# Optimization experiments

Measured on AMD Instinct MI355X. Metric: run time of the kernel, lower is better.

Reference implementation:

```python
import jax, jax.numpy as jnp
import numpy as np

B, LP, LQ, H = 32, 2048, 512, 1024

def setup_inputs() -> dict:
    key = jax.random.key(0)
    k1, k2, k3, k4 = jax.random.split(key, 4)
    p_encode = jax.random.normal(k1, (B, LP, H), dtype=jnp.float32)
    q_encode = jax.random.normal(k2, (B, LQ, H), dtype=jnp.float32)
    # nn.Linear(H, H): weight [out, in], bias [out]
    bound = 1.0 / np.sqrt(H)
    G_weight = jax.random.uniform(k3, (H, H), dtype=jnp.float32, minval=-bound, maxval=bound)
    G_bias = jax.random.uniform(k4, (H,), dtype=jnp.float32, minval=-bound, maxval=bound)
    return {"p_encode": p_encode, "q_encode": q_encode, "G_weight": G_weight, "G_bias": G_bias}

def reference(p_encode, q_encode, G_weight, G_bias):
    # q_project = transpose(G(q_encode), -2, -1): [B, H, LQ]
    q_proj = jnp.einsum('bqh,oh->bqo', q_encode, G_weight) + G_bias  # [B, LQ, H]
    # att_matrix = bmm(p_encode, q_project^T): [B, LP, LQ]
    att = jnp.einsum('bph,bqh->bpq', p_encode, q_proj)
    # m_p = softmax over LQ (dim=-1) @ q_encode -> [B, LP, H]
    m_p = jnp.einsum('bpq,bqh->bph', jax.nn.softmax(att, axis=-1), q_encode)
    # m_q = softmax over LP (dim=-2), transposed, @ p_encode -> [B, LQ, H]
    m_q = jnp.einsum('bpq,bph->bqh', jax.nn.softmax(att, axis=-2), p_encode)
    return (m_p, m_q)
```

## Files before the change

### kernel.cpp

```cpp
#include <hip/hip_runtime.h>

typedef _Float16 half_t;
typedef _Float16 f16x8 __attribute__((ext_vector_type(8)));
typedef _Float16 f16x4 __attribute__((ext_vector_type(4)));
typedef float    f32x4 __attribute__((ext_vector_type(4)));
typedef float    f32x16 __attribute__((ext_vector_type(16)));

typedef const __attribute__((address_space(1))) void cg_void;
typedef __attribute__((address_space(3))) void lds_void;

#define BB 32
#define LP 2048
#define LQ 512
#define HH 1024

enum { M_QPROJ = 0, M_OUT32 = 1 };

__global__ void cvt16_k(const float* __restrict__ w, half_t* __restrict__ o) {
  long i = ((long)blockIdx.x * 256 + threadIdx.x) * 4;
  f32x4 v = *(const f32x4*)(w + i);
  f16x4 h;
  h[0] = (half_t)v[0]; h[1] = (half_t)v[1]; h[2] = (half_t)v[2]; h[3] = (half_t)v[3];
  *(f16x4*)(o + i) = h;
}

__global__ __launch_bounds__(256) void cvt2_k(const float* __restrict__ qe,
                                              half_t* __restrict__ q16o,
                                              half_t* __restrict__ qT16o,
                                              const float* __restrict__ pe,
                                              half_t* __restrict__ p16o,
                                              half_t* __restrict__ pT16o) {
  __shared__ half_t tile[64 * 64];
  const int byg = blockIdx.y;
  const float* in; half_t* rm; half_t* tr; int R, r0;
  if (byg < 8) { in = qe; rm = q16o; tr = qT16o; R = LQ; r0 = byg * 64; }
  else         { in = pe; rm = p16o; tr = pT16o; R = LP; r0 = (byg - 8) * 64; }
  const int C = HH;
  const long zb = blockIdx.z;
  const float* src = in + zb * (long)R * C;
  half_t* dstT = tr + zb * (long)C * R;
  half_t* dstR = rm + zb * (long)R * C;
  const int c0 = blockIdx.x * 64;
  const int t = threadIdx.x;
  const int cl = (t & 15) * 4;
  const int rl = t >> 4;
#pragma unroll
  for (int rr = 0; rr < 4; rr++) {
    int r = rr * 16 + rl;
    f32x4 v = *(const f32x4*)(src + (long)(r0 + r) * C + c0 + cl);
    f16x4 h;
#pragma unroll
    for (int j = 0; j < 4; j++) {
      h[j] = (half_t)v[j];
      int c = cl + j;
      tile[c * 64 + (r ^ (((c >> 3) & 7) << 3))] = h[j];
    }
    *(f16x4*)(dstR + (long)(r0 + r) * C + c0 + cl) = h;
  }
  __syncthreads();
  const int c = t >> 2;
  const int rch = (t & 3) * 16;
  const int m = (c >> 3) & 7;
  const int B0 = c * 64 + (rch ^ ((m << 3) & 48));
  const int hi = (m & 1) << 3;
  f16x8 g0 = *(const f16x8*)&tile[B0 + hi];
  f16x8 g1 = *(const f16x8*)&tile[B0 + (8 ^ hi)];
  half_t* dp = dstT + (long)(c0 + c) * R + r0 + rch;
  *(f16x8*)dp = g0;
  *(f16x8*)(dp + 8) = g1;
}

__global__ __launch_bounds__(256) void cfin_k(const float* __restrict__ pmg,
                                              const float* __restrict__ psg,
                                              float* __restrict__ cmax,
                                              float* __restrict__ cinv) {
  long i = (long)blockIdx.x * 256 + threadIdx.x;
  long b = i / LQ, q = i - b * LQ;
  const float* mp = pmg + (b * 16) * LQ + q;
  const float* sp = psg + (b * 16) * LQ + q;
  float m = -3e38f, s = 0.f;
#pragma unroll
  for (int t = 0; t < 16; t++) {
    float mm = mp[(long)t * LQ], ss = sp[(long)t * LQ];
    float nm = fmaxf(m, mm);
    s = s * __expf(m - nm) + ss * __expf(mm - nm);
    m = nm;
  }
  cmax[i] = m;
  cinv[i] = 1.f / s;
}

__global__ __launch_bounds__(256) void pq_k(const half_t* __restrict__ E,
                                            half_t* __restrict__ out,
                                            const float* __restrict__ pmg,
                                            const float* __restrict__ cmax,
                                            const float* __restrict__ cinv) {
  __shared__ half_t tile[64 * 64];
  const long zb = blockIdx.z;
  const half_t* src = E + zb * (long)LP * LQ;
  half_t* dst = out + zb * (long)LQ * LP;
  const int r0 = blockIdx.y * 64, c0 = blockIdx.x * 64;
  const int tIdx = r0 >> 7;
  const int t = threadIdx.x;
  const int cl = (t & 15) * 4;
  const int rl = t >> 4;
  f32x4 tm = *(const f32x4*)(pmg + ((long)zb * 16 + tIdx) * LQ + c0 + cl);
  f32x4 cm = *(const f32x4*)(cmax + (long)zb * LQ + c0 + cl);
  f32x4 ci = *(const f32x4*)(cinv + (long)zb * LQ + c0 + cl);
  float sc[4];
#pragma unroll
  for (int j = 0; j < 4; j++) sc[j] = __expf(tm[j] - cm[j]) * ci[j];
#pragma unroll
  for (int rr = 0; rr < 4; rr++) {
    int r = rr * 16 + rl;
    f16x4 v = *(const f16x4*)(src + (long)(r0 + r) * LQ + c0 + cl);
#pragma unroll
    for (int j = 0; j < 4; j++) {
      float x = (float)v[j] * sc[j];
      int c = cl + j;
      tile[c * 64 + (r ^ (((c >> 3) & 7) << 3))] = (half_t)x;
    }
  }
  __syncthreads();
  const int c = t >> 2;
  const int rch = (t & 3) * 16;
  const int m = (c >> 3) & 7;
  const int B0 = c * 64 + (rch ^ ((m << 3) & 48));
  const int hi = (m & 1) << 3;
  f16x8 g0 = *(const f16x8*)&tile[B0 + hi];
  f16x8 g1 = *(const f16x8*)&tile[B0 + (8 ^ hi)];
  half_t* dp = dst + (long)(c0 + c) * LP + r0 + rch;
  *(f16x8*)dp = g0;
  *(f16x8*)(dp + 8) = g1;
}

template<int ROWS>
__device__ __forceinline__ void stage_op(const half_t* src, int ld,
                                         half_t* lds_base, int wid, int lane) {
  const int goff = (((lane & 3) ^ ((lane >> 3) & 3)) << 3);
#pragma unroll
  for (int j = 0; j < ROWS / 128; ++j) {
    int row = j * 128 + wid * 16 + (lane >> 2);
    const half_t* g = src + (long)row * ld + goff;
    __builtin_amdgcn_global_load_lds((cg_void*)g,
        (lds_void*)(lds_base + j * 4096 + wid * 512), 16, 0, 0);
  }
}

__device__ __forceinline__ void xcd_swz(long lid, long nwg, long& out) {
  const long q8 = nwg >> 3, r8 = nwg & 7;
  const long xcd = lid & 7, rest = lid >> 3;
  out = (xcd < r8 ? xcd * (q8 + 1) : r8 * (q8 + 1) + (xcd - r8) * q8) + rest;
}

__global__ __launch_bounds__(512, 2) void attf_k(
    const half_t* __restrict__ Ap, const half_t* __restrict__ Bp,
    half_t* __restrict__ PpO, half_t* __restrict__ EO,
    float* __restrict__ pmg, float* __restrict__ psg) {
  __shared__ __align__(16) half_t As[3 * 4096];
  __shared__ __align__(16) half_t Bs[3 * 16384];
  __shared__ float rmL[4][128];
  __shared__ float cmL[2][512];
  __shared__ float rsL[4][128];
  __shared__ float csL[2][512];

  const int nby = gridDim.y;
  long lid;
  xcd_swz(blockIdx.y + (long)nby * blockIdx.z, (long)nby * gridDim.z, lid);
  const int by = (int)(lid % nby);
  const int bz = (int)(lid / nby);

  const int t0 = threadIdx.x;
  const int lane = t0 & 63;
  const int wid = t0 >> 6;
  const int wm = wid >> 2, wn = wid & 3;
  const int m0 = by * 128;

  const half_t* Abase = Ap + ((long)bz * LP + m0) * HH;
  const half_t* Bbase = Bp + (long)bz * LQ * HH;

  const int c5 = lane & 31, hi = lane >> 5;
  const int sx = (c5 >> 1) & 3;
  const int ofs0 = c5 * 32 + ((hi ^ sx) << 3);
  const int ofs1 = c5 * 32 + (((2 | hi) ^ sx) << 3);

  f32x16 acc[2][4] = {};
  const int NT = HH / 32;

#pragma unroll
  for (int tt = 0; tt < 2; ++tt) {
    stage_op<128>(Abase + tt * 32, HH, As + tt * 4096, wid, lane);
    stage_op<512>(Bbase + tt * 32, HH, Bs + tt * 16384, wid, lane);
  }

  for (int t = 0; t < NT; ++t) {
    if (t + 1 < NT) asm volatile("s_waitcnt vmcnt(5)" ::: "memory");
    else            asm volatile("s_waitcnt vmcnt(0)" ::: "memory");
    __builtin_amdgcn_s_barrier();
    asm volatile("" ::: "memory");

    const half_t* Au = As + (t % 3) * 4096;
    const half_t* Bu = Bs + (t % 3) * 16384;
    f16x8 af[2][2], bf[4][2];
#pragma unroll
    for (int mf = 0; mf < 2; ++mf) {
      const half_t* p = Au + (wm * 64 + mf * 32) * 32;
      af[mf][0] = *(const f16x8*)(p + ofs0);
      af[mf][1] = *(const f16x8*)(p + ofs1);
    }
#pragma unroll
    for (int nf = 0; nf < 4; ++nf) {
      const half_t* p = Bu + (wn * 128 + nf * 32) * 32;
      bf[nf][0] = *(const f16x8*)(p + ofs0);
      bf[nf][1] = *(const f16x8*)(p + ofs1);
    }
    if (t + 2 < NT) {
      const int u2 = (t + 2) % 3;
      stage_op<128>(Abase + (t + 2) * 32, HH, As + u2 * 4096, wid, lane);
      stage_op<512>(Bbase + (t + 2) * 32, HH, Bs + u2 * 16384, wid, lane);
    }
    __builtin_amdgcn_s_setprio(1);
#pragma unroll
    for (int mf = 0; mf < 2; ++mf)
#pragma unroll
      for (int nf = 0; nf < 4; ++nf) {
        acc[mf][nf] = __builtin_amdgcn_mfma_f32_32x32x16_f16(af[mf][0], bf[nf][0], acc[mf][nf], 0, 0, 0);
        acc[mf][nf] = __builtin_amdgcn_mfma_f32_32x32x16_f16(af[mf][1], bf[nf][1], acc[mf][nf], 0, 0, 0);
      }
    __builtin_amdgcn_s_setprio(0);
  }

  float rmv[2][16], cmv[4];
#pragma unroll
  for (int m = 0; m < 2; ++m)
#pragma unroll
    for (int r = 0; r < 16; ++r) {
      float v = fmaxf(fmaxf(acc[m][0][r], acc[m][1][r]), fmaxf(acc[m][2][r], acc[m][3][r]));
#pragma unroll
      for (int o = 1; o < 32; o <<= 1) v = fmaxf(v, __shfl_xor(v, o, 64));
      rmv[m][r] = v;
    }
#pragma unroll
  for (int n = 0; n < 4; ++n) {
    float v = acc[0][n][0];
#pragma unroll
    for (int m = 0; m < 2; ++m)
#pragma unroll
      for (int r = 0; r < 16; ++r) v = fmaxf(v, acc[m][n][r]);
    v = fmaxf(v, __shfl_xor(v, 32, 64));
    cmv[n] = v;
  }
  if (c5 < 16) {
#pragma unroll
    for (int m = 0; m < 2; ++m)
      rmL[wn][wm * 64 + m * 32 + (c5 & 3) + 8 * (c5 >> 2) + 4 * hi] = rmv[m][c5];
  }
  if (hi == 0) {
#pragma unroll
    for (int n = 0; n < 4; ++n) cmL[wm][wn * 128 + n * 32 + c5] = cmv[n];
  }
  __syncthreads();
  if (t0 < 128)
    rmL[0][t0] = fmaxf(fmaxf(rmL[0][t0], rmL[1][t0]), fmaxf(rmL[2][t0], rmL[3][t0]));
  {
    float cm2 = fmaxf(cmL[0][t0 & 511], cmL[1][t0 & 511]);
    cmL[0][t0 & 511] = cm2;
    pmg[((long)bz * 16 + by) * LQ + (t0 & 511)] = cm2;
  }
  __syncthreads();
#pragma unroll
  for (int m = 0; m < 2; ++m)
#pragma unroll
    for (int r = 0; r < 16; ++r)
      rmv[m][r] = rmL[0][wm * 64 + m * 32 + (r & 3) + 8 * (r >> 2) + 4 * hi];
#pragma unroll
  for (int n = 0; n < 4; ++n) cmv[n] = cmL[0][wn * 128 + n * 32 + c5];

  half_t* EB = EO + (long)bz * LP * LQ;
  float csW[4] = {0.f, 0.f, 0.f, 0.f};
  float rowS[2][16];
#pragma unroll
  for (int m = 0; m < 2; ++m)
#pragma unroll
    for (int r = 0; r < 16; ++r) {
      long grow = (long)(m0 + wm * 64 + m * 32 + (r & 3) + 8 * (r >> 2) + 4 * hi) * LQ;
      float s = 0.f;
#pragma unroll
      for (int n = 0; n < 4; ++n) {
        float a = acc[m][n][r];
        float e = __expf(a - cmv[n]);
        float p = __expf(a - rmv[m][r]);
        csW[n] += e;
        EB[grow + wn * 128 + n * 32 + c5] = (half_t)e;
        acc[m][n][r] = p;
        s += p;
      }
#pragma unroll
      for (int o = 1; o < 32; o <<= 1) s += __shfl_xor(s, o, 64);
      rowS[m][r] = s;
    }
#pragma unroll
  for (int n = 0; n < 4; ++n) csW[n] += __shfl_xor(csW[n], 32, 64);
  if (c5 < 16) {
#pragma unroll
    for (int m = 0; m < 2; ++m)
      rsL[wn][wm * 64 + m * 32 + (c5 & 3) + 8 * (c5 >> 2) + 4 * hi] = rowS[m][c5];
  }
  if (hi == 0) {
#pragma unroll
    for (int n = 0; n < 4; ++n) csL[wm][wn * 128 + n * 32 + c5] = csW[n];
  }
  __syncthreads();
  if (t0 < 128)
    rsL[0][t0] = 1.f / (rsL[0][t0] + rsL[1][t0] + rsL[2][t0] + rsL[3][t0]);
  psg[((long)bz * 16 + by) * LQ + (t0 & 511)] = csL[0][t0 & 511] + csL[1][t0 & 511];
  __syncthreads();

  half_t* PpB = PpO + (long)bz * LP * LQ;
#pragma unroll
  for (int m = 0; m < 2; ++m)
#pragma unroll
    for (int r = 0; r < 16; ++r) {
      int row = wm * 64 + m * 32 + (r & 3) + 8 * (r >> 2) + 4 * hi;
      long grow = (long)(m0 + row) * LQ;
      float ri = rsL[0][row];
#pragma unroll
      for (int n = 0; n < 4; ++n)
        PpB[grow + wn * 128 + n * 32 + c5] = (half_t)(acc[m][n][r] * ri);
    }
}

__device__ __forceinline__ void stage_half(const half_t* src, int ld, int k0,
                                           half_t* slot, int half_id, int wid, int lane) {
#pragma unroll
  for (int j = 0; j < 2; ++j) {
    int c = j * 512 + wid * 64 + lane;
    int lr = c >> 3, sl = c & 7;
    int gr = (lr & 63) + half_id * 64 + (lr >> 6) * 128;
    const half_t* g = src + (long)gr * ld + k0 + (((sl ^ (lr & 7))) << 3);
    __builtin_amdgcn_global_load_lds((cg_void*)g,
        (lds_void*)(slot + j * 4096 + wid * 512), 16, 0, 0);
  }
}

__device__ __forceinline__ void stage_s(int s, const half_t* Ab, const half_t* Bb,
                                        int lda, int ldb, half_t* lds, int NT,
                                        int wid, int lane) {
  int ts = s >> 2;
  if (ts >= NT) return;
  int kind = s & 3;
  half_t* slot = lds + (s & 7) * 8192;
  int k0 = ts * 64;
  if (kind == 0)      stage_half(Ab, lda, k0, slot, 0, wid, lane);
  else if (kind == 1) stage_half(Bb, ldb, k0, slot, 0, wid, lane);
  else if (kind == 2) stage_half(Bb, ldb, k0, slot, 1, wid, lane);
  else                stage_half(Ab, lda, k0, slot, 1, wid, lane);
}

template<int MODE>
__device__ __forceinline__ void core8p(const half_t* __restrict__ Ab,
                                       const half_t* __restrict__ Bb,
                                       void* __restrict__ cB,
                                       const float* __restrict__ biasB,
                                       int lda, int ldb, int ldc, int K,
                                       half_t* lds) {
  const int t0 = threadIdx.x;
  const int lane = t0 & 63;
  const int wid = t0 >> 6;
  const int wm = wid >> 2, wn = wid & 3;
  const int fr = lane & 15, fs = lane >> 4;

  f32x4 acc[8][4] = {};
  const int NT = K >> 6;

#pragma unroll
  for (int s = 0; s < 6; ++s) stage_s(s, Ab, Bb, lda, ldb, lds, NT, wid, lane);
  asm volatile("s_waitcnt vmcnt(6)" ::: "memory");
  __builtin_amdgcn_s_barrier();
  asm volatile("" ::: "memory");

  for (int t = 0; t < NT; ++t) {
    const int base4 = 4 * t;
    const half_t* slotA0 = lds + ((base4) & 7) * 8192;
    const half_t* slotB0 = lds + ((base4 + 1) & 7) * 8192;
    const half_t* slotB1 = lds + ((base4 + 2) & 7) * 8192;
    const half_t* slotA1 = lds + ((base4 + 3) & 7) * 8192;
    f16x8 bf[4][2];
#pragma unroll
    for (int p = 0; p < 4; ++p) {
      f16x8 af[2][2];
      const half_t* aslot = (p < 2) ? slotA0 : slotA1;
      const int lrbase = wm * 64 + (p & 1) * 32;
#pragma unroll
      for (int i = 0; i < 2; ++i) {
        int lr = lrbase + i * 16 + fr;
#pragma unroll
        for (int kh = 0; kh < 2; ++kh)
          af[i][kh] = *(const f16x8*)&aslot[lr * 64 + (((fs + 4 * kh) ^ (lr & 7)) << 3)];
      }
      if (p == 0) {
        const half_t* bslot = (wn & 1) ? slotB1 : slotB0;
#pragma unroll
        for (int nf = 0; nf < 4; ++nf) {
          int lr = (wn >> 1) * 64 + nf * 16 + fr;
#pragma unroll
          for (int kh = 0; kh < 2; ++kh)
            bf[nf][kh] = *(const f16x8*)&bslot[lr * 64 + (((fs + 4 * kh) ^ (lr & 7)) << 3)];
        }
      }
      stage_s(base4 + p + 6, Ab, Bb, lda, ldb, lds, NT, wid, lane);
      if (t + 2 < NT) {
        asm volatile("s_waitcnt vmcnt(6)" ::: "memory");
      } else if (t + 2 == NT) {
        if (p < 2)       asm volatile("s_waitcnt vmcnt(6)" ::: "memory");
        else if (p == 2) asm volatile("s_waitcnt vmcnt(4)" ::: "memory");
        else             asm volatile("s_waitcnt vmcnt(2)" ::: "memory");
      } else {
        asm volatile("s_waitcnt vmcnt(0)" ::: "memory");
      }
      __builtin_amdgcn_s_barrier();
      asm volatile("s_waitcnt lgkmcnt(0)" ::: "memory");
      __builtin_amdgcn_sched_barrier(0);
      __builtin_amdgcn_s_setprio(1);
#pragma unroll
      for (int kh = 0; kh < 2; ++kh)
#pragma unroll
        for (int i = 0; i < 2; ++i)
#pragma unroll
          for (int nf = 0; nf < 4; ++nf)
            acc[p * 2 + i][nf] =
                __builtin_amdgcn_mfma_f32_16x16x32_f16(af[i][kh], bf[nf][kh], acc[p * 2 + i][nf], 0, 0, 0);
      __builtin_amdgcn_s_setprio(0);
      __builtin_amdgcn_s_barrier();
      asm volatile("" ::: "memory");
    }
  }

  const int r0 = fs * 4;
#pragma unroll
  for (int nf = 0; nf < 4; ++nf) {
    int col = wn * 64 + nf * 16 + fr;
    float bv = 0.f;
    if constexpr (MODE == M_QPROJ) bv = biasB[col];
#pragma unroll
    for (int mf = 0; mf < 8; ++mf) {
      int row = wm * 128 + (mf >> 2) * 64 + ((mf >> 1) & 1) * 32 + (mf & 1) * 16 + r0;
#pragma unroll
      for (int j = 0; j < 4; j++) {
        if constexpr (MODE == M_QPROJ)
          ((half_t*)cB)[(long)(row + j) * ldc + col] = (half_t)(acc[mf][nf][j] + bv);
        else
          ((float*)cB)[(long)(row + j) * ldc + col] = acc[mf][nf][j];
      }
    }
  }
}

__global__ __launch_bounds__(512, 1) void gemmq_k(const half_t* __restrict__ q16,
                                                  const half_t* __restrict__ w16,
                                                  half_t* __restrict__ qpj,
                                                  const float* __restrict__ Gb) {
  __shared__ __align__(16) half_t lds[8 * 8192];
  long lid;
  xcd_swz(blockIdx.x + 4L * blockIdx.y, 4L * gridDim.y, lid);
  const int bx = (int)(lid % 4);
  const int by = (int)(lid / 4);
  core8p<M_QPROJ>(q16 + (long)(by * 256) * HH,
                  w16 + (long)(bx * 256) * HH,
                  qpj + (long)(by * 256) * HH + bx * 256,
                  Gb + bx * 256, HH, HH, HH, HH, lds);
}

__global__ __launch_bounds__(512, 1) void gemm2_k(
    const half_t* __restrict__ Pp, const half_t* __restrict__ qT16, float* __restrict__ m_p,
    const half_t* __restrict__ Pq, const half_t* __restrict__ pT16, float* __restrict__ m_q) {
  __shared__ __align__(16) half_t lds[8 * 8192];
  long lid;
  xcd_swz(blockIdx.x + 4L * (blockIdx.y + 10L * blockIdx.z), 4L * 10 * 32, lid);
  const int bx = (int)(lid % 4);
  const long tmp = lid / 4;
  const int by = (int)(tmp % 10);
  const int bz = (int)(tmp / 10);

  if (by < 2) {
    core8p<M_OUT32>(Pq + (long)bz * LQ * LP + (long)(by * 256) * LP,
                    pT16 + (long)bz * HH * LP + (long)(bx * 256) * LP,
                    m_q + (long)bz * LQ * HH + (long)(by * 256) * HH + bx * 256,
                    nullptr, LP, LP, HH, LP, lds);
  } else {
    const int py = by - 2;
    core8p<M_OUT32>(Pp + (long)bz * LP * LQ + (long)(py * 256) * LQ,
                    qT16 + (long)bz * HH * LQ + (long)(bx * 256) * LQ,
                    m_p + (long)bz * LP * HH + (long)(py * 256) * HH + bx * 256,
                    nullptr, LQ, LQ, HH, LQ, lds);
  }
}

extern "C" void kernel_launch(void* const* d_in, const int* in_sizes, int n_in,
                              void* d_out, int out_size, void* d_ws, size_t ws_size,
                              hipStream_t stream) {
  const float* p_enc = (const float*)d_in[0];
  const float* q_enc = (const float*)d_in[1];
  const float* Gw    = (const float*)d_in[2];
  const float* Gb    = (const float*)d_in[3];
  float* m_p = (float*)d_out;
  float* m_q = m_p + (long)BB * LP * HH;

  half_t* w16   = (half_t*)d_ws;
  half_t* q16   = w16 + (long)HH * HH;
  half_t* qT16  = q16 + (long)BB * LQ * HH;
  half_t* qpj16 = qT16 + (long)BB * HH * LQ;
  half_t* p16   = qpj16 + (long)BB * LQ * HH;
  half_t* pT16  = p16 + (long)BB * LP * HH;
  half_t* Pp    = pT16 + (long)BB * HH * LP;
  half_t* Ebuf  = Pp + (long)BB * LP * LQ;
  half_t* Pq    = Ebuf + (long)BB * LP * LQ;
  float*  cmaxb = (float*)(Pq + (long)BB * LQ * LP);
  float*  cinvb = cmaxb + (long)BB * LQ;
  float*  pmg   = cinvb + (long)BB * LQ;
  float*  psg   = pmg + (long)BB * 16 * LQ;

  cvt16_k<<<HH * HH / 1024, 256, 0, stream>>>(Gw, w16);

  cvt2_k<<<dim3(HH / 64, 40, BB), 256, 0, stream>>>(q_enc, q16, qT16, p_enc, p16, pT16);

  gemmq_k<<<dim3(4, 64, 1), 512, 0, stream>>>(q16, w16, qpj16, Gb);

  attf_k<<<dim3(1, LP / 128, BB), 512, 0, stream>>>(p16, qpj16, Pp, Ebuf, pmg, psg);

  cfin_k<<<BB * LQ / 256, 256, 0, stream>>>(pmg, psg, cmaxb, cinvb);
  pq_k<<<dim3(LQ / 64, LP / 64, BB), 256, 0, stream>>>(Ebuf, Pq, pmg, cmaxb, cinvb);

  gemm2_k<<<dim3(4, 10, BB), 512, 0, stream>>>(Pp, qT16, m_p, Pq, pT16, m_q);
}
```

Measured before the change: 498.4 us.

## Fuse column-softmax finalize into transpose kernel with per-block row loop

New measurement: 517.4 us. +3.8%, slower.

```diff
diff --git a/kernel.cpp b/kernel.cpp
--- a/kernel.cpp
+++ b/kernel.cpp
@@ -70,68 +70,69 @@
   *(f16x8*)(dp + 8) = g1;
 }
 
-__global__ __launch_bounds__(256) void cfin_k(const float* __restrict__ pmg,
-                                              const float* __restrict__ psg,
-                                              float* __restrict__ cmax,
-                                              float* __restrict__ cinv) {
-  long i = (long)blockIdx.x * 256 + threadIdx.x;
-  long b = i / LQ, q = i - b * LQ;
-  const float* mp = pmg + (b * 16) * LQ + q;
-  const float* sp = psg + (b * 16) * LQ + q;
-  float m = -3e38f, s = 0.f;
-#pragma unroll
-  for (int t = 0; t < 16; t++) {
-    float mm = mp[(long)t * LQ], ss = sp[(long)t * LQ];
-    float nm = fmaxf(m, mm);
-    s = s * __expf(m - nm) + ss * __expf(mm - nm);
-    m = nm;
-  }
-  cmax[i] = m;
-  cinv[i] = 1.f / s;
-}
-
-__global__ __launch_bounds__(256) void pq_k(const half_t* __restrict__ E,
-                                            half_t* __restrict__ out,
-                                            const float* __restrict__ pmg,
-                                            const float* __restrict__ cmax,
-                                            const float* __restrict__ cinv) {
+__global__ __launch_bounds__(256) void pqf_k(const half_t* __restrict__ E,
+                                             half_t* __restrict__ out,
+                                             const float* __restrict__ pmg,
+                                             const float* __restrict__ psg) {
   __shared__ half_t tile[64 * 64];
   const long zb = blockIdx.z;
-  const half_t* src = E + zb * (long)LP * LQ;
-  half_t* dst = out + zb * (long)LQ * LP;
-  const int r0 = blockIdx.y * 64, c0 = blockIdx.x * 64;
-  const int tIdx = r0 >> 7;
+  const int c0 = blockIdx.x * 64;
   const int t = threadIdx.x;
   const int cl = (t & 15) * 4;
   const int rl = t >> 4;
-  f32x4 tm = *(const f32x4*)(pmg + ((long)zb * 16 + tIdx) * LQ + c0 + cl);
-  f32x4 cm = *(const f32x4*)(cmax + (long)zb * LQ + c0 + cl);
-  f32x4 ci = *(const f32x4*)(cinv + (long)zb * LQ + c0 + cl);
-  float sc[4];
-#pragma unroll
-  for (int j = 0; j < 4; j++) sc[j] = __expf(tm[j] - cm[j]) * ci[j];
-#pragma unroll
-  for (int rr = 0; rr < 4; rr++) {
-    int r = rr * 16 + rl;
-    f16x4 v = *(const f16x4*)(src + (long)(r0 + r) * LQ + c0 + cl);
-#pragma unroll
-    for (int j = 0; j < 4; j++) {
-      float x = (float)v[j] * sc[j];
-      int c = cl + j;
-      tile[c * 64 + (r ^ (((c >> 3) & 7) << 3))] = (half_t)x;
-    }
-  }
-  __syncthreads();
+
+  const float* mpb = pmg + (long)zb * 16 * LQ + c0 + cl;
+  const float* spb = psg + (long)zb * 16 * LQ + c0 + cl;
+  float m4[4] = {-3e38f, -3e38f, -3e38f, -3e38f}, s4[4] = {0.f, 0.f, 0.f, 0.f};
+#pragma unroll
+  for (int tt = 0; tt < 16; ++tt) {
+    f32x4 mm = *(const f32x4*)(mpb + (long)tt * LQ);
+    f32x4 ss = *(const f32x4*)(spb + (long)tt * LQ);
+#pragma unroll
+    for (int j = 0; j < 4; ++j) {
+      float nm = fmaxf(m4[j], mm[j]);
+      s4[j] = s4[j] * __expf(m4[j] - nm) + ss[j] * __expf(mm[j] - nm);
+      m4[j] = nm;
+    }
+  }
+  float ci4[4];
+#pragma unroll
+  for (int j = 0; j < 4; ++j) ci4[j] = 1.f / s4[j];
+
+  const half_t* src = E + zb * (long)LP * LQ;
+  half_t* dst = out + zb * (long)LQ * LP;
   const int c = t >> 2;
   const int rch = (t & 3) * 16;
-  const int m = (c >> 3) & 7;
-  const int B0 = c * 64 + (rch ^ ((m << 3) & 48));
-  const int hi = (m & 1) << 3;
-  f16x8 g0 = *(const f16x8*)&tile[B0 + hi];
-  f16x8 g1 = *(const f16x8*)&tile[B0 + (8 ^ hi)];
-  half_t* dp = dst + (long)(c0 + c) * LP + r0 + rch;
-  *(f16x8*)dp = g0;
-  *(f16x8*)(dp + 8) = g1;
+  const int mswz = (c >> 3) & 7;
+  const int B0 = c * 64 + (rch ^ ((mswz << 3) & 48));
+  const int hi = (mswz & 1) << 3;
+
+  for (int rt = 0; rt < LP / 64; ++rt) {
+    const int r0 = rt * 64;
+    const int tIdx = r0 >> 7;
+    f32x4 tm = *(const f32x4*)(mpb + (long)tIdx * LQ);
+    float sc[4];
+#pragma unroll
+    for (int j = 0; j < 4; ++j) sc[j] = __expf(tm[j] - m4[j]) * ci4[j];
+#pragma unroll
+    for (int rr = 0; rr < 4; rr++) {
+      int r = rr * 16 + rl;
+      f16x4 v = *(const f16x4*)(src + (long)(r0 + r) * LQ + c0 + cl);
+#pragma unroll
+      for (int j = 0; j < 4; j++) {
+        float x = (float)v[j] * sc[j];
+        int cc = cl + j;
+        tile[cc * 64 + (r ^ (((cc >> 3) & 7) << 3))] = (half_t)x;
+      }
+    }
+    __syncthreads();
+    f16x8 g0 = *(const f16x8*)&tile[B0 + hi];
+    f16x8 g1 = *(const f16x8*)&tile[B0 + (8 ^ hi)];
+    half_t* dp = dst + (long)(c0 + c) * LP + r0 + rch;
+    *(f16x8*)dp = g0;
+    *(f16x8*)(dp + 8) = g1;
+    __syncthreads();
+  }
 }
 
 template<int ROWS>
@@ -515,9 +516,7 @@
   half_t* Pp    = pT16 + (long)BB * HH * LP;
   half_t* Ebuf  = Pp + (long)BB * LP * LQ;
   half_t* Pq    = Ebuf + (long)BB * LP * LQ;
-  float*  cmaxb = (float*)(Pq + (long)BB * LQ * LP);
-  float*  cinvb = cmaxb + (long)BB * LQ;
-  float*  pmg   = cinvb + (long)BB * LQ;
+  float*  pmg   = (float*)(Pq + (long)BB * LQ * LP);
   float*  psg   = pmg + (long)BB * 16 * LQ;
 
   cvt16_k<<<HH * HH / 1024, 256, 0, stream>>>(Gw, w16);
@@ -528,8 +527,7 @@
 
   attf_k<<<dim3(1, LP / 128, BB), 512, 0, stream>>>(p16, qpj16, Pp, Ebuf, pmg, psg);
 
-  cfin_k<<<BB * LQ / 256, 256, 0, stream>>>(pmg, psg, cmaxb, cinvb);
-  pq_k<<<dim3(LQ / 64, LP / 64, BB), 256, 0, stream>>>(Ebuf, Pq, pmg, cmaxb, cinvb);
+  pqf_k<<<dim3(LQ / 64, 1, BB), 256, 0, stream>>>(Ebuf, Pq, pmg, psg);
 
   gemm2_k<<<dim3(4, 10, BB), 512, 0, stream>>>(Pp, qT16, m_p, Pq, pT16, m_q);
 }
```
